# Optimization experiments

Measured on AMD Instinct MI355X. Metric: run time of the kernel, lower is better.

The kernel has to match this reference:

```python
import jax, jax.numpy as jnp
import numpy as np

SIGMA = 0.4            # gaussian geodesic kernel width (class default)
B, N_IN, N_OUT, C, K = 2, 163842, 40962, 128, 7  # icosphere rank 7 -> rank 6, valence-7 candidates


def setup_inputs() -> dict:
    key = jax.random.key(0)
    k_x, k_p, k_o, k_c, k_d = jax.random.split(key, 5)
    x = jax.random.normal(k_x, (B, N_IN, C), dtype=jnp.float32)
    parent_idx = jax.random.randint(k_p, (N_IN,), 0, N_OUT)
    omega = jax.random.uniform(k_o, (N_IN,), dtype=jnp.float32, minval=0.5, maxval=1.5)
    omega = omega / omega.mean()          # matches omega / omega.mean() in __init__
    cand_idx = jax.random.randint(k_c, (N_IN, K), 0, N_OUT)
    cand_mask = jnp.ones((N_IN, K), dtype=jnp.float32)
    delta = jax.random.uniform(k_d, (N_IN, K), dtype=jnp.float32, minval=0.0, maxval=0.5)
    return dict(x=x, omega=omega, delta=delta, cand_mask=cand_mask,
                parent_idx=parent_idx, cand_idx=cand_idx)


def reference(x, omega, delta, cand_mask, parent_idx, cand_idx):
    # --- AreaWeightedDownsample: weight, scatter-add to coarse nodes, normalize ---
    weighted = x * omega[None, :, None]                        # [B, N_in, C]
    down = jnp.zeros((x.shape[0], N_OUT, x.shape[2]), x.dtype)
    down = down.at[:, parent_idx].add(weighted)                # scatter_add over node dim
    denom = jnp.zeros((N_OUT,), x.dtype).at[parent_idx].add(omega)
    down = down / jnp.clip(denom, 1e-8)[None, :, None]         # [B, N_out, C]
    # --- GeodesicKernelUpsample: gather K coarse candidates, gaussian geodesic weights ---
    w = jnp.exp(-(delta * delta) / (2.0 * SIGMA * SIGMA)) * cand_mask   # [N_in, K]
    w = w / jnp.clip(w.sum(axis=-1, keepdims=True), 1e-8)
    gathered = down[:, cand_idx]                               # [B, N_in, K, C]
    return jnp.einsum('nk,bnkc->bnc', w, gathered)             # [B, N_in, C]
```

## Files before the change

### kernel.cpp

```cpp
#include <hip/hip_runtime.h>
#include <hip/hip_bf16.h>

#define B_SZ   2
#define N_IN   163842
#define N_OUT  40962
#define C_DIM  128
#define K_CAND 7
#define INV_2SIG2 3.125f

#define SCAN_B 256
#define NBLK_SCAN ((N_OUT + SCAN_B - 1) / SCAN_B)

__global__ __launch_bounds__(256) void count_kernel(
    const int* __restrict__ parent, int* __restrict__ count)
{
    int n = blockIdx.x * 256 + threadIdx.x;
    if (n < N_IN) atomicAdd(&count[parent[n]], 1);
}

__global__ __launch_bounds__(SCAN_B) void scan1_kernel(
    const int* __restrict__ count, int* __restrict__ offs, int* __restrict__ bsum)
{
    __shared__ int sh[SCAN_B];
    const int t = threadIdx.x;
    const int j = blockIdx.x * SCAN_B + t;
    const int c = (j < N_OUT) ? count[j] : 0;
    sh[t] = c;
    __syncthreads();
    for (int off = 1; off < SCAN_B; off <<= 1) {
        int v = (t >= off) ? sh[t - off] : 0;
        __syncthreads();
        sh[t] += v;
        __syncthreads();
    }
    if (j < N_OUT) offs[j] = sh[t] - c;
    if (t == SCAN_B - 1) bsum[blockIdx.x] = sh[t];
}

__global__ __launch_bounds__(SCAN_B) void scan2_kernel(
    const int* __restrict__ bsum, int* __restrict__ bbase)
{
    __shared__ int sh[SCAN_B];
    const int t = threadIdx.x;
    const int s = (t < NBLK_SCAN) ? bsum[t] : 0;
    sh[t] = s;
    __syncthreads();
    for (int off = 1; off < SCAN_B; off <<= 1) {
        int v = (t >= off) ? sh[t - off] : 0;
        __syncthreads();
        sh[t] += v;
        __syncthreads();
    }
    if (t < NBLK_SCAN) bbase[t] = sh[t] - s;
}

__global__ __launch_bounds__(SCAN_B) void scan3_kernel(
    int* __restrict__ offs, const int* __restrict__ bbase)
{
    const int j = blockIdx.x * SCAN_B + threadIdx.x;
    if (j < N_OUT && blockIdx.x > 0) offs[j] += bbase[blockIdx.x];
}

__global__ __launch_bounds__(256) void fill_kernel(
    const int* __restrict__ parent, const int* __restrict__ offs,
    int* __restrict__ cursor, int* __restrict__ perm)
{
    int n = blockIdx.x * 256 + threadIdx.x;
    if (n < N_IN) {
        int p = parent[n];
        int pos = offs[p] + atomicAdd(&cursor[p], 1);
        perm[pos] = n;
    }
}

__global__ __launch_bounds__(256) void reduce_kernel(
    const float* __restrict__ x,
    const float* __restrict__ omega,
    const int*   __restrict__ offs,
    const int*   __restrict__ perm,
    __hip_bfloat16* __restrict__ down)
{
    const int sub = threadIdx.x >> 5;
    const int l   = threadIdx.x & 31;
    const int p   = blockIdx.x * 8 + sub;
    if (p >= N_OUT) return;

    const int beg = offs[p];
    const int end = (p + 1 < N_OUT) ? offs[p + 1] : N_IN;

    const float4* x4 = (const float4*)x;
    float4 a0 = make_float4(0.f, 0.f, 0.f, 0.f);
    float4 a1 = make_float4(0.f, 0.f, 0.f, 0.f);
    float ds = 0.f;

    for (int i = beg; i < end; ++i) {
        const int n = perm[i];
        const float om = omega[n];
        ds += om;
        const float4 v0 = x4[(size_t)n * 32 + l];
        const float4 v1 = x4[((size_t)N_IN + n) * 32 + l];
        a0.x = fmaf(v0.x, om, a0.x); a0.y = fmaf(v0.y, om, a0.y);
        a0.z = fmaf(v0.z, om, a0.z); a0.w = fmaf(v0.w, om, a0.w);
        a1.x = fmaf(v1.x, om, a1.x); a1.y = fmaf(v1.y, om, a1.y);
        a1.z = fmaf(v1.z, om, a1.z); a1.w = fmaf(v1.w, om, a1.w);
    }
    const float inv = 1.f / fmaxf(ds, 1e-8f);

    __hip_bfloat162* d2 = (__hip_bfloat162*)down;
    __hip_bfloat162 h;
    h.x = __float2bfloat16(a0.x * inv); h.y = __float2bfloat16(a0.y * inv);
    d2[(size_t)p * 64 + l * 2] = h;
    h.x = __float2bfloat16(a0.z * inv); h.y = __float2bfloat16(a0.w * inv);
    d2[(size_t)p * 64 + l * 2 + 1] = h;
    h.x = __float2bfloat16(a1.x * inv); h.y = __float2bfloat16(a1.y * inv);
    d2[((size_t)N_OUT + p) * 64 + l * 2] = h;
    h.x = __float2bfloat16(a1.z * inv); h.y = __float2bfloat16(a1.w * inv);
    d2[((size_t)N_OUT + p) * 64 + l * 2 + 1] = h;
}

__global__ __launch_bounds__(256) void gather_kernel(
    const float* __restrict__ delta,
    const float* __restrict__ cand_mask,
    const int*   __restrict__ cand_idx,
    const __hip_bfloat16* __restrict__ down,
    float* __restrict__ out)
{
    const int g    = threadIdx.x >> 6;
    const int lane = threadIdx.x & 63;
    const int n    = blockIdx.x * 4 + g;

    __shared__ float w_sh[4][8];
    __shared__ float coef_sh[4][8];
    __shared__ int   idx_sh[4][8];

    if (n < N_IN && lane < K_CAND) {
        const float d = delta[(size_t)n * K_CAND + lane];
        w_sh[g][lane] = __expf(-d * d * INV_2SIG2) *
                        cand_mask[(size_t)n * K_CAND + lane];
        idx_sh[g][lane] = cand_idx[(size_t)n * K_CAND + lane];
    }
    __syncthreads();
    if (n < N_IN && lane < K_CAND) {
        float s = 0.f;
        #pragma unroll
        for (int k = 0; k < K_CAND; ++k) s += w_sh[g][k];
        coef_sh[g][lane] = w_sh[g][lane] / fmaxf(s, 1e-8f);
    }
    __syncthreads();

    if (n >= N_IN) return;

    const __hip_bfloat162* d2 = (const __hip_bfloat162*)down;
    float2 acc0 = make_float2(0.f, 0.f);
    float2 acc1 = make_float2(0.f, 0.f);
    #pragma unroll
    for (int k = 0; k < K_CAND; ++k) {
        const float cf = coef_sh[g][k];
        const int   p  = idx_sh[g][k];
        const __hip_bfloat162 v0 = d2[(size_t)p * 64 + lane];
        const __hip_bfloat162 v1 = d2[((size_t)N_OUT + p) * 64 + lane];
        acc0.x = fmaf(cf, __bfloat162float(v0.x), acc0.x);
        acc0.y = fmaf(cf, __bfloat162float(v0.y), acc0.y);
        acc1.x = fmaf(cf, __bfloat162float(v1.x), acc1.x);
        acc1.y = fmaf(cf, __bfloat162float(v1.y), acc1.y);
    }
    float2* o2 = (float2*)out;
    o2[(size_t)n * 64 + lane]          = acc0;
    o2[((size_t)N_IN + n) * 64 + lane] = acc1;
}

extern "C" void kernel_launch(void* const* d_in, const int* in_sizes, int n_in,
                              void* d_out, int out_size, void* d_ws, size_t ws_size,
                              hipStream_t stream) {
    const float* x         = (const float*)d_in[0];
    const float* omega     = (const float*)d_in[1];
    const float* delta     = (const float*)d_in[2];
    const float* cand_mask = (const float*)d_in[3];
    const int*   parent    = (const int*)d_in[4];
    const int*   cand_idx  = (const int*)d_in[5];
    float* out = (float*)d_out;

    __hip_bfloat16* down = (__hip_bfloat16*)d_ws;
    int* ints   = (int*)(down + (size_t)B_SZ * N_OUT * C_DIM);
    int* count  = ints;
    int* cursor = ints + N_OUT;
    int* offs   = ints + 2 * N_OUT;
    int* perm   = ints + 3 * N_OUT;
    int* bsum   = perm + N_IN;
    int* bbase  = bsum + 256;

    hipMemsetAsync(ints, 0, (size_t)2 * N_OUT * sizeof(int), stream);

    const int nblk = (N_IN + 255) / 256;
    count_kernel<<<nblk, 256, 0, stream>>>(parent, count);
    scan1_kernel<<<NBLK_SCAN, SCAN_B, 0, stream>>>(count, offs, bsum);
    scan2_kernel<<<1, SCAN_B, 0, stream>>>(bsum, bbase);
    scan3_kernel<<<NBLK_SCAN, SCAN_B, 0, stream>>>(offs, bbase);
    fill_kernel<<<nblk, 256, 0, stream>>>(parent, offs, cursor, perm);
    reduce_kernel<<<(N_OUT + 7) / 8, 256, 0, stream>>>(x, omega, offs, perm, down);
    gather_kernel<<<(N_IN + 3) / 4, 256, 0, stream>>>(
        delta, cand_mask, cand_idx, down, out);
}
```

Baseline: 415.1 us.

## Fuse scan into single block, shuffle-broadcast reduce/gather, vectorize bf16 access

Replaces the three-kernel prefix scan with one single-block scan and reuses the count buffer as the fill cursor via atomicSub, removing launches and a memset. The reduce kernel uses a full wave per coarse node, splitting batches by half-wave and broadcasting perm/omega through shuffles. The gather kernel computes normalized weights with shuffles instead of shared memory and barriers, and uses 8-byte bf16 loads and nontemporal 16-byte stores. The single-block scan serializes work on one CU, and summation order within buckets changes.

```diff
diff --git a/kernel.cpp b/kernel.cpp
--- a/kernel.cpp
+++ b/kernel.cpp
@@ -8,8 +8,15 @@
 #define K_CAND 7
 #define INV_2SIG2 3.125f
 
-#define SCAN_B 256
-#define NBLK_SCAN ((N_OUT + SCAN_B - 1) / SCAN_B)
+typedef float f32x4 __attribute__((ext_vector_type(4)));
+
+__device__ __forceinline__ float bf2f(unsigned short u) {
+    return __uint_as_float((unsigned)u << 16);
+}
+__device__ __forceinline__ unsigned short f2bf(float f) {
+    unsigned u = __float_as_uint(f);
+    return (unsigned short)((u + 0x7fffu + ((u >> 16) & 1u)) >> 16);
+}
 
 __global__ __launch_bounds__(256) void count_kernel(
     const int* __restrict__ parent, int* __restrict__ count)
@@ -18,57 +25,47 @@
     if (n < N_IN) atomicAdd(&count[parent[n]], 1);
 }
 
-__global__ __launch_bounds__(SCAN_B) void scan1_kernel(
-    const int* __restrict__ count, int* __restrict__ offs, int* __restrict__ bsum)
+#define SCAN_T 1024
+#define PER_T  41
+__global__ __launch_bounds__(SCAN_T) void scan_kernel(
+    const int* __restrict__ count, int* __restrict__ offs)
 {
-    __shared__ int sh[SCAN_B];
+    __shared__ int sh[SCAN_T];
     const int t = threadIdx.x;
-    const int j = blockIdx.x * SCAN_B + t;
-    const int c = (j < N_OUT) ? count[j] : 0;
-    sh[t] = c;
+    const int base = t * PER_T;
+    int local[PER_T];
+    int sum = 0;
+    #pragma unroll
+    for (int i = 0; i < PER_T; ++i) {
+        const int j = base + i;
+        const int c = (j < N_OUT) ? count[j] : 0;
+        local[i] = sum;
+        sum += c;
+    }
+    sh[t] = sum;
     __syncthreads();
-    for (int off = 1; off < SCAN_B; off <<= 1) {
+    for (int off = 1; off < SCAN_T; off <<= 1) {
         int v = (t >= off) ? sh[t - off] : 0;
         __syncthreads();
         sh[t] += v;
         __syncthreads();
     }
-    if (j < N_OUT) offs[j] = sh[t] - c;
-    if (t == SCAN_B - 1) bsum[blockIdx.x] = sh[t];
-}
-
-__global__ __launch_bounds__(SCAN_B) void scan2_kernel(
-    const int* __restrict__ bsum, int* __restrict__ bbase)
-{
-    __shared__ int sh[SCAN_B];
-    const int t = threadIdx.x;
-    const int s = (t < NBLK_SCAN) ? bsum[t] : 0;
-    sh[t] = s;
-    __syncthreads();
-    for (int off = 1; off < SCAN_B; off <<= 1) {
-        int v = (t >= off) ? sh[t - off] : 0;
-        __syncthreads();
-        sh[t] += v;
-        __syncthreads();
+    const int ebase = sh[t] - sum;
+    #pragma unroll
+    for (int i = 0; i < PER_T; ++i) {
+        const int j = base + i;
+        if (j < N_OUT) offs[j] = ebase + local[i];
     }
-    if (t < NBLK_SCAN) bbase[t] = sh[t] - s;
-}
-
-__global__ __launch_bounds__(SCAN_B) void scan3_kernel(
-    int* __restrict__ offs, const int* __restrict__ bbase)
-{
-    const int j = blockIdx.x * SCAN_B + threadIdx.x;
-    if (j < N_OUT && blockIdx.x > 0) offs[j] += bbase[blockIdx.x];
 }
 
 __global__ __launch_bounds__(256) void fill_kernel(
     const int* __restrict__ parent, const int* __restrict__ offs,
-    int* __restrict__ cursor, int* __restrict__ perm)
+    int* __restrict__ count, int* __restrict__ perm)
 {
     int n = blockIdx.x * 256 + threadIdx.x;
     if (n < N_IN) {
-        int p = parent[n];
-        int pos = offs[p] + atomicAdd(&cursor[p], 1);
+        const int p = parent[n];
+        const int pos = offs[p] + atomicSub(&count[p], 1) - 1;
         perm[pos] = n;
     }
 }
@@ -80,42 +77,50 @@
     const int*   __restrict__ perm,
     __hip_bfloat16* __restrict__ down)
 {
-    const int sub = threadIdx.x >> 5;
-    const int l   = threadIdx.x & 31;
-    const int p   = blockIdx.x * 8 + sub;
+    const int wid  = threadIdx.x >> 6;
+    const int lane = threadIdx.x & 63;
+    const int p = blockIdx.x * 4 + wid;
     if (p >= N_OUT) return;
 
     const int beg = offs[p];
     const int end = (p + 1 < N_OUT) ? offs[p + 1] : N_IN;
+    const int cnt = end - beg;
 
-    const float4* x4 = (const float4*)x;
-    float4 a0 = make_float4(0.f, 0.f, 0.f, 0.f);
-    float4 a1 = make_float4(0.f, 0.f, 0.f, 0.f);
+    const int half = lane >> 5;
+    const int l    = lane & 31;
+    const f32x4* x4 = (const f32x4*)x;
+    const size_t bofs = (size_t)half * N_IN * 32;
+
+    f32x4 acc = {0.f, 0.f, 0.f, 0.f};
     float ds = 0.f;
 
-    for (int i = beg; i < end; ++i) {
-        const int n = perm[i];
-        const float om = omega[n];
-        ds += om;
-        const float4 v0 = x4[(size_t)n * 32 + l];
-        const float4 v1 = x4[((size_t)N_IN + n) * 32 + l];
-        a0.x = fmaf(v0.x, om, a0.x); a0.y = fmaf(v0.y, om, a0.y);
-        a0.z = fmaf(v0.z, om, a0.z); a0.w = fmaf(v0.w, om, a0.w);
-        a1.x = fmaf(v1.x, om, a1.x); a1.y = fmaf(v1.y, om, a1.y);
-        a1.z = fmaf(v1.z, om, a1.z); a1.w = fmaf(v1.w, om, a1.w);
+    for (int cbase = 0; cbase < cnt; cbase += 64) {
+        const int m = min(64, cnt - cbase);
+        int   myn  = 0;
+        float myom = 0.f;
+        if (lane < m) {
+            myn  = perm[beg + cbase + lane];
+            myom = omega[myn];
+        }
+        for (int j = 0; j < m; ++j) {
+            const int   n  = __shfl(myn,  j);
+            const float om = __shfl(myom, j);
+            ds += om;
+            const f32x4 v = __builtin_nontemporal_load(&x4[bofs + (size_t)n * 32 + l]);
+            acc.x = fmaf(v.x, om, acc.x);
+            acc.y = fmaf(v.y, om, acc.y);
+            acc.z = fmaf(v.z, om, acc.z);
+            acc.w = fmaf(v.w, om, acc.w);
+        }
     }
     const float inv = 1.f / fmaxf(ds, 1e-8f);
 
-    __hip_bfloat162* d2 = (__hip_bfloat162*)down;
-    __hip_bfloat162 h;
-    h.x = __float2bfloat16(a0.x * inv); h.y = __float2bfloat16(a0.y * inv);
-    d2[(size_t)p * 64 + l * 2] = h;
-    h.x = __float2bfloat16(a0.z * inv); h.y = __float2bfloat16(a0.w * inv);
-    d2[(size_t)p * 64 + l * 2 + 1] = h;
-    h.x = __float2bfloat16(a1.x * inv); h.y = __float2bfloat16(a1.y * inv);
-    d2[((size_t)N_OUT + p) * 64 + l * 2] = h;
-    h.x = __float2bfloat16(a1.z * inv); h.y = __float2bfloat16(a1.w * inv);
-    d2[((size_t)N_OUT + p) * 64 + l * 2 + 1] = h;
+    ushort4 hh;
+    hh.x = f2bf(acc.x * inv);
+    hh.y = f2bf(acc.y * inv);
+    hh.z = f2bf(acc.z * inv);
+    hh.w = f2bf(acc.w * inv);
+    ((ushort4*)down)[((size_t)half * N_OUT + p) * 32 + l] = hh;
 }
 
 __global__ __launch_bounds__(256) void gather_kernel(
@@ -125,48 +130,43 @@
     const __hip_bfloat16* __restrict__ down,
     float* __restrict__ out)
 {
-    const int g    = threadIdx.x >> 6;
+    const int wid  = threadIdx.x >> 6;
     const int lane = threadIdx.x & 63;
-    const int n    = blockIdx.x * 4 + g;
-
-    __shared__ float w_sh[4][8];
-    __shared__ float coef_sh[4][8];
-    __shared__ int   idx_sh[4][8];
-
-    if (n < N_IN && lane < K_CAND) {
-        const float d = delta[(size_t)n * K_CAND + lane];
-        w_sh[g][lane] = __expf(-d * d * INV_2SIG2) *
-                        cand_mask[(size_t)n * K_CAND + lane];
-        idx_sh[g][lane] = cand_idx[(size_t)n * K_CAND + lane];
-    }
-    __syncthreads();
-    if (n < N_IN && lane < K_CAND) {
-        float s = 0.f;
-        #pragma unroll
-        for (int k = 0; k < K_CAND; ++k) s += w_sh[g][k];
-        coef_sh[g][lane] = w_sh[g][lane] / fmaxf(s, 1e-8f);
-    }
-    __syncthreads();
-
+    const int n = blockIdx.x * 4 + wid;
     if (n >= N_IN) return;
 
-    const __hip_bfloat162* d2 = (const __hip_bfloat162*)down;
-    float2 acc0 = make_float2(0.f, 0.f);
-    float2 acc1 = make_float2(0.f, 0.f);
+    float w = 0.f;
+    int pidx = 0;
+    if (lane < K_CAND) {
+        const float d   = __builtin_nontemporal_load(&delta[(size_t)n * K_CAND + lane]);
+        const float msk = __builtin_nontemporal_load(&cand_mask[(size_t)n * K_CAND + lane]);
+        pidx = __builtin_nontemporal_load(&cand_idx[(size_t)n * K_CAND + lane]);
+        w = __expf(-d * d * INV_2SIG2) * msk;
+    }
+    float s = w;
+    s += __shfl_xor(s, 1);
+    s += __shfl_xor(s, 2);
+    s += __shfl_xor(s, 4);
+    const float coef = w / fmaxf(s, 1e-8f);
+
+    const int half = lane >> 5;
+    const int l    = lane & 31;
+    const ushort4* d4 = (const ushort4*)down;
+    const size_t bofs = (size_t)half * N_OUT * 32;
+
+    f32x4 acc = {0.f, 0.f, 0.f, 0.f};
     #pragma unroll
     for (int k = 0; k < K_CAND; ++k) {
-        const float cf = coef_sh[g][k];
-        const int   p  = idx_sh[g][k];
-        const __hip_bfloat162 v0 = d2[(size_t)p * 64 + lane];
-        const __hip_bfloat162 v1 = d2[((size_t)N_OUT + p) * 64 + lane];
-        acc0.x = fmaf(cf, __bfloat162float(v0.x), acc0.x);
-        acc0.y = fmaf(cf, __bfloat162float(v0.y), acc0.y);
-        acc1.x = fmaf(cf, __bfloat162float(v1.x), acc1.x);
-        acc1.y = fmaf(cf, __bfloat162float(v1.y), acc1.y);
+        const float cf = __shfl(coef, k);
+        const int   p  = __shfl(pidx, k);
+        const ushort4 v = d4[bofs + (size_t)p * 32 + l];
+        acc.x = fmaf(cf, bf2f(v.x), acc.x);
+        acc.y = fmaf(cf, bf2f(v.y), acc.y);
+        acc.z = fmaf(cf, bf2f(v.z), acc.z);
+        acc.w = fmaf(cf, bf2f(v.w), acc.w);
     }
-    float2* o2 = (float2*)out;
-    o2[(size_t)n * 64 + lane]          = acc0;
-    o2[((size_t)N_IN + n) * 64 + lane] = acc1;
+    f32x4* o4 = (f32x4*)out;
+    __builtin_nontemporal_store(acc, &o4[((size_t)half * N_IN + n) * 32 + l]);
 }
 
 extern "C" void kernel_launch(void* const* d_in, const int* in_sizes, int n_in,
@@ -181,23 +181,17 @@
     float* out = (float*)d_out;
 
     __hip_bfloat16* down = (__hip_bfloat16*)d_ws;
-    int* ints   = (int*)(down + (size_t)B_SZ * N_OUT * C_DIM);
-    int* count  = ints;
-    int* cursor = ints + N_OUT;
-    int* offs   = ints + 2 * N_OUT;
-    int* perm   = ints + 3 * N_OUT;
-    int* bsum   = perm + N_IN;
-    int* bbase  = bsum + 256;
+    int* count = (int*)(down + (size_t)B_SZ * N_OUT * C_DIM);
+    int* offs  = count + N_OUT;
+    int* perm  = offs + N_OUT;
 
-    hipMemsetAsync(ints, 0, (size_t)2 * N_OUT * sizeof(int), stream);
+    hipMemsetAsync(count, 0, (size_t)N_OUT * sizeof(int), stream);
 
     const int nblk = (N_IN + 255) / 256;
     count_kernel<<<nblk, 256, 0, stream>>>(parent, count);
-    scan1_kernel<<<NBLK_SCAN, SCAN_B, 0, stream>>>(count, offs, bsum);
-    scan2_kernel<<<1, SCAN_B, 0, stream>>>(bsum, bbase);
-    scan3_kernel<<<NBLK_SCAN, SCAN_B, 0, stream>>>(offs, bbase);
-    fill_kernel<<<nblk, 256, 0, stream>>>(parent, offs, cursor, perm);
-    reduce_kernel<<<(N_OUT + 7) / 8, 256, 0, stream>>>(x, omega, offs, perm, down);
+    scan_kernel<<<1, SCAN_T, 0, stream>>>(count, offs);
+    fill_kernel<<<nblk, 256, 0, stream>>>(parent, offs, count, perm);
+    reduce_kernel<<<(N_OUT + 3) / 4, 256, 0, stream>>>(x, omega, offs, perm, down);
     gather_kernel<<<(N_IN + 3) / 4, 256, 0, stream>>>(
         delta, cand_mask, cand_idx, down, out);
 }
```

After: 430.7 us. 3.8% more time.
